# Kernel tuning notes

Hardware: AMD Instinct MI355X
Metric: run time of the kernel (lower is better)

## Reference

```python
import jax, jax.numpy as jnp
import numpy as np

B, N, NC, D, H = 2, 8192, 512, 512, 16
HD = D // H            # 32
SCALE = HD ** -0.5
EPS = 1e-6


def setup_inputs() -> dict:
    key = jax.random.key(0)
    k0, k1, k2, k3, k4 = jax.random.split(key, 5)
    return {
        "x": jax.random.normal(k0, (B, N, D), dtype=jnp.float32),
        "clusters": jax.random.normal(k1, (B, NC, D), dtype=jnp.float32),
        "Wq": jax.random.normal(k2, (D, D), dtype=jnp.float32) * 0.02,
        "Wkv": jax.random.normal(k3, (D, 2 * D), dtype=jnp.float32) * 0.02,
        "Wout": jax.random.normal(k4, (D, D), dtype=jnp.float32) * 0.02,
    }


def reference(x, clusters, Wq, Wkv, Wout):
    # projections (torch Linear without bias == matmul with weight)
    q = clusters @ Wq                      # [b, nc, d]
    kv = x @ Wkv                           # [b, n, 2d]
    # split heads: 'b n (h d) -> b h n d' and 'b n (k h d) -> k b h n d'
    q = q.reshape(B, NC, H, HD).transpose(0, 2, 1, 3)        # [b, h, nc, hd]
    kv = kv.reshape(B, N, 2, H, HD)
    k = kv[:, :, 0].transpose(0, 2, 1, 3)                    # [b, h, n, hd]
    v = kv[:, :, 1].transpose(0, 2, 1, 3)                    # [b, h, n, hd]

    attn = jnp.einsum('bhqd,bhkd->bhqk', q, k) * SCALE       # [b, h, nc, n]
    # 'soft' assignment: softmax over the CLUSTER (query) axis, dim=-2
    attn = jax.nn.softmax(attn, axis=-2)
    token_sizes = attn.sum(-1)                               # [b, h, nc]
    attn = attn / (token_sizes[..., None] + EPS)
    token_sizes = token_sizes.mean(axis=1)                   # [b, nc]

    out = jnp.einsum('bhqk,bhkd->bhqd', attn, v)             # [b, h, nc, hd]
    out = out.transpose(0, 2, 1, 3).reshape(B, NC, D)        # [b, nc, d]
    out = out @ Wout
    return out, token_sizes
```

## Files before the change

### kernel.cpp

```cpp
#include <hip/hip_runtime.h>
#include <hip/hip_bf16.h>

#define B_ 2
#define N_ 8192
#define NC_ 512
#define D_ 512
#define H_ 16
#define HD_ 32
#define SCALE_ 0.17677669529663687f
#define LOG2E_ 1.4426950408889634f
#define EPS_ 1e-6f
#define NCHUNK 32
#define CHUNK (N_ / NCHUNK)

typedef __attribute__((ext_vector_type(8))) short bf16x8_t;
typedef __attribute__((ext_vector_type(4))) short bf16x4_t;
typedef __attribute__((ext_vector_type(4))) float f32x4_t;

static __device__ __forceinline__ short f2bf(float f) {
    unsigned u = __float_as_uint(f);
    unsigned r = (u + 0x7FFFu + ((u >> 16) & 1u)) >> 16;
    return (short)r;
}

static __device__ __forceinline__ float fast_exp2(float x) {
#if __has_builtin(__builtin_amdgcn_exp2f)
    return __builtin_amdgcn_exp2f(x);
#else
    float r; asm("v_exp_f32 %0, %1" : "=v"(r) : "v"(x)); return r;
#endif
}

static __device__ __forceinline__ unsigned pack_trunc(float lo, float hi) {
    return __builtin_amdgcn_perm(__float_as_uint(hi), __float_as_uint(lo), 0x07060302u);
}

static __device__ __forceinline__ float bf2f(short s) {
    return __uint_as_float((unsigned)(unsigned short)s << 16);
}

static __device__ __forceinline__ void gload_lds16(const short* g, void* l) {
    __builtin_amdgcn_global_load_lds(
        (const __attribute__((address_space(1))) void*)g,
        (__attribute__((address_space(3))) void*)l, 16, 0, 0);
}

__global__ __launch_bounds__(256) void prep_kernel(
    const float* __restrict__ x, short* __restrict__ x_bf, int na8,
    const float* __restrict__ clusters, short* __restrict__ cl_bf,
    const float* __restrict__ Wq, const float* __restrict__ Wkv,
    const float* __restrict__ Wout,
    short* __restrict__ WqT, short* __restrict__ WkvT, short* __restrict__ WoutT)
{
    __shared__ short t[32][34];
    const int bid = blockIdx.x;
    if (bid < 4352) {
        int i8 = bid * 256 + threadIdx.x;
        const float* src; short* dst;
        if (i8 < na8) { src = x + (size_t)i8 * 8; dst = x_bf + (size_t)i8 * 8; }
        else { size_t o = (size_t)(i8 - na8) * 8; src = clusters + o; dst = cl_bf + o; }
        float4 v0 = *(const float4*)src;
        float4 v1 = *(const float4*)(src + 4);
        bf16x8_t p = {f2bf(v0.x), f2bf(v0.y), f2bf(v0.z), f2bf(v0.w),
                      f2bf(v1.x), f2bf(v1.y), f2bf(v1.z), f2bf(v1.w)};
        *(bf16x8_t*)dst = p;
        return;
    }
    const int idx = bid - 4352;
    const int bz = idx >> 9, rem = idx & 511;
    const int byy = rem >> 5, bxx = rem & 31;
    const float* src; short* dst; int ncols;
    if (bz == 0)      { src = Wq;   dst = WqT;   ncols = 512; }
    else if (bz == 1) { src = Wkv;  dst = WkvT;  ncols = 1024; }
    else              { src = Wout; dst = WoutT; ncols = 512; }
    if (bxx * 32 >= ncols) return;

    const int c0 = bxx * 32, r0 = byy * 32;
    const int tc = threadIdx.x & 31, tr = threadIdx.x >> 5;
#pragma unroll
    for (int i = 0; i < 4; i++) {
        int r = tr + i * 8;
        t[tc][r] = f2bf(src[(size_t)(r0 + r) * ncols + c0 + tc]);
    }
    __syncthreads();
#pragma unroll
    for (int i = 0; i < 4; i++) {
        int outr = tr + i * 8;
        dst[(size_t)(c0 + outr) * 512 + r0 + tc] = t[outr][tc];
    }
}

__global__ __launch_bounds__(256) void gemm_kvq_kernel(
    const short* __restrict__ x_bf, const short* __restrict__ WkvT,
    short* __restrict__ kvb,
    const short* __restrict__ cl_bf, const short* __restrict__ WqT,
    short* __restrict__ qb)
{
    __shared__ short As[2][128 * 32];
    __shared__ short Bs[2][128 * 32];

    const int tid = threadIdx.x;
    const int wid = tid >> 6, lane = tid & 63;
    const int l16 = lane & 15, lg = lane >> 4;
    const int wr = (wid >> 1) * 64, wc = (wid & 1) * 64;
    const int K = D_;

    const short* A; const short* BT; short* C; int N; float oscale; int bx, by;
    if (blockIdx.x < 1024) {
        int swz = (blockIdx.x & 7) * 128 + (blockIdx.x >> 3);
        bx = swz & 7; by = swz >> 3;
        A = x_bf; BT = WkvT; C = kvb; N = 2 * D_; oscale = 1.0f;
    } else {
        int r = blockIdx.x - 1024;
        bx = r & 3; by = r >> 2;
        A = cl_bf; BT = WqT; C = qb; N = D_; oscale = SCALE_ * LOG2E_;
    }

    const f32x4_t zero4 = {0.f, 0.f, 0.f, 0.f};
    f32x4_t acc[4][4];
#pragma unroll
    for (int i = 0; i < 4; i++)
#pragma unroll
        for (int j = 0; j < 4; j++) acc[i][j] = zero4;

    const short* aptr = A + (size_t)(by * 128 + wid * 16 + (lane >> 2)) * K + (lane & 3) * 8;
    const short* bptr = BT + (size_t)(bx * 128 + wid * 16 + (lane >> 2)) * K + (lane & 3) * 8;
    char* al0 = (char*)As[0] + wid * 1024;
    char* al1 = (char*)As[1] + wid * 1024;
    char* bl0 = (char*)Bs[0] + wid * 1024;
    char* bl1 = (char*)Bs[1] + wid * 1024;
    const size_t rstep = (size_t)64 * K;

    for (int kt = 0; kt < K; kt += 64) {
        gload_lds16(aptr + kt, al0);
        gload_lds16(aptr + rstep + kt, al0 + 4096);
        gload_lds16(aptr + kt + 32, al1);
        gload_lds16(aptr + rstep + kt + 32, al1 + 4096);
        gload_lds16(bptr + kt, bl0);
        gload_lds16(bptr + rstep + kt, bl0 + 4096);
        gload_lds16(bptr + kt + 32, bl1);
        gload_lds16(bptr + rstep + kt + 32, bl1 + 4096);
        __syncthreads();

#pragma unroll
        for (int sub = 0; sub < 2; sub++) {
            bf16x8_t bfr[4];
#pragma unroll
            for (int nf = 0; nf < 4; nf++)
                bfr[nf] = *(const bf16x8_t*)&Bs[sub][(wc + nf * 16 + l16) * 32 + lg * 8];
#pragma unroll
            for (int mf = 0; mf < 4; mf++) {
                bf16x8_t afr = *(const bf16x8_t*)&As[sub][(wr + mf * 16 + l16) * 32 + lg * 8];
#pragma unroll
                for (int nf = 0; nf < 4; nf++)
                    acc[mf][nf] = __builtin_amdgcn_mfma_f32_16x16x32_bf16(
                        afr, bfr[nf], acc[mf][nf], 0, 0, 0);
            }
        }
        __syncthreads();
    }

#pragma unroll
    for (int mf = 0; mf < 4; mf++) {
#pragma unroll
        for (int nf = 0; nf < 4; nf++) {
            int row0 = by * 128 + wr + mf * 16 + lg * 4;
            int col  = bx * 128 + wc + nf * 16 + l16;
#pragma unroll
            for (int r = 0; r < 4; r++)
                C[(size_t)(row0 + r) * N + col] = f2bf(acc[mf][nf][r] * oscale);
        }
    }
}

__global__ __launch_bounds__(256) void gemm_out_kernel(
    const short* __restrict__ A, const short* __restrict__ BT,
    float* __restrict__ C)
{
    __shared__ short As[2][128 * 32];
    __shared__ short Bs[2][128 * 32];

    const int tid = threadIdx.x;
    const int wid = tid >> 6, lane = tid & 63;
    const int l16 = lane & 15, lg = lane >> 4;
    const int wr = (wid >> 1) * 64, wc = (wid & 1) * 64;
    const int K = D_, N = D_;

    const int nwg = gridDim.x * gridDim.y;
    const int flat = blockIdx.y * gridDim.x + blockIdx.x;
    const int swz = (flat & 7) * (nwg >> 3) + (flat >> 3);
    const int bx = swz % gridDim.x, by = swz / gridDim.x;

    const f32x4_t zero4 = {0.f, 0.f, 0.f, 0.f};
    f32x4_t acc[4][4];
#pragma unroll
    for (int i = 0; i < 4; i++)
#pragma unroll
        for (int j = 0; j < 4; j++) acc[i][j] = zero4;

    const short* aptr = A + (size_t)(by * 128 + wid * 16 + (lane >> 2)) * K + (lane & 3) * 8;
    const short* bptr = BT + (size_t)(bx * 128 + wid * 16 + (lane >> 2)) * K + (lane & 3) * 8;
    char* al0 = (char*)As[0] + wid * 1024;
    char* al1 = (char*)As[1] + wid * 1024;
    char* bl0 = (char*)Bs[0] + wid * 1024;
    char* bl1 = (char*)Bs[1] + wid * 1024;
    const size_t rstep = (size_t)64 * K;

    for (int kt = 0; kt < K; kt += 64) {
        gload_lds16(aptr + kt, al0);
        gload_lds16(aptr + rstep + kt, al0 + 4096);
        gload_lds16(aptr + kt + 32, al1);
        gload_lds16(aptr + rstep + kt + 32, al1 + 4096);
        gload_lds16(bptr + kt, bl0);
        gload_lds16(bptr + rstep + kt, bl0 + 4096);
        gload_lds16(bptr + kt + 32, bl1);
        gload_lds16(bptr + rstep + kt + 32, bl1 + 4096);
        __syncthreads();

#pragma unroll
        for (int sub = 0; sub < 2; sub++) {
            bf16x8_t bfr[4];
#pragma unroll
            for (int nf = 0; nf < 4; nf++)
                bfr[nf] = *(const bf16x8_t*)&Bs[sub][(wc + nf * 16 + l16) * 32 + lg * 8];
#pragma unroll
            for (int mf = 0; mf < 4; mf++) {
                bf16x8_t afr = *(const bf16x8_t*)&As[sub][(wr + mf * 16 + l16) * 32 + lg * 8];
#pragma unroll
                for (int nf = 0; nf < 4; nf++)
                    acc[mf][nf] = __builtin_amdgcn_mfma_f32_16x16x32_bf16(
                        afr, bfr[nf], acc[mf][nf], 0, 0, 0);
            }
        }
        __syncthreads();
    }

#pragma unroll
    for (int mf = 0; mf < 4; mf++) {
#pragma unroll
        for (int nf = 0; nf < 4; nf++) {
            int row0 = by * 128 + wr + mf * 16 + lg * 4;
            int col  = bx * 128 + wc + nf * 16 + l16;
#pragma unroll
            for (int r = 0; r < 4; r++)
                C[(size_t)(row0 + r) * N + col] = acc[mf][nf][r];
        }
    }
}

__global__ __launch_bounds__(256) void attn_kernel(
    const short* __restrict__ qb,
    const short* __restrict__ kvb,
    short* __restrict__ out_part,
    float* __restrict__ ts_part)
{
    const int chunk = blockIdx.x, h = blockIdx.y, b = blockIdx.z;
    const int tid = threadIdx.x, wid = tid >> 6, lane = tid & 63;
    const int l16 = lane & 15, lg = lane >> 4;

    __shared__ short P_lds[512 * 32];
    __shared__ short v_t[2][32][40];
    __shared__ float reds[2][4][32];

    bf16x8_t qf[8];
#pragma unroll
    for (int mf = 0; mf < 8; mf++) {
        int row = wid * 128 + mf * 16 + l16;
        qf[mf] = *(const bf16x8_t*)&qb[(size_t)(b * NC_ + row) * D_ + h * HD_ + lg * 8];
    }

    const f32x4_t zero4 = {0.f, 0.f, 0.f, 0.f};
    f32x4_t oacc[8][2], tsacc[8];
#pragma unroll
    for (int mf = 0; mf < 8; mf++) {
        oacc[mf][0] = zero4; oacc[mf][1] = zero4; tsacc[mf] = zero4;
    }

    const short* kptr = kvb + (size_t)(b * N_ + chunk * CHUNK + l16) * (2 * D_) + h * HD_ + lg * 8;
    const int skey = tid >> 3, sd0 = (tid & 7) * 4;
    const short* vptr = kvb + (size_t)(b * N_ + chunk * CHUNK + skey) * (2 * D_) + D_ + h * HD_ + sd0;
    char* Pb = (char*)P_lds;

    bf16x8_t kf0 = *(const bf16x8_t*)(kptr);
    bf16x8_t kf1 = *(const bf16x8_t*)(kptr + 16 * (2 * D_));
    bf16x4_t vv  = *(const bf16x4_t*)(vptr);

    for (int kt = 0; kt < CHUNK / 32; kt++) {
        const int cur = kt & 1;

        v_t[cur][sd0 + 0][skey] = vv[0];
        v_t[cur][sd0 + 1][skey] = vv[1];
        v_t[cur][sd0 + 2][skey] = vv[2];
        v_t[cur][sd0 + 3][skey] = vv[3];

#pragma unroll
        for (int half = 0; half < 2; half++) {
            f32x4_t s[8];
            bf16x8_t kf = half ? kf1 : kf0;
#pragma unroll
            for (int mf = 0; mf < 8; mf++)
                s[mf] = __builtin_amdgcn_mfma_f32_16x16x32_bf16(qf[mf], kf, zero4, 0, 0, 0);

            const int kbyte = (l16 & 7) * 2;
            const int ku = (l16 >> 3) + half * 2;
            float sl = 0.f;
#pragma unroll
            for (int mf = 0; mf < 8; mf++) {
#pragma unroll
                for (int r = 0; r < 4; r++) {
                    float e = fast_exp2(s[mf][r]);
                    sl += e;
                    int row = wid * 128 + mf * 16 + lg * 4 + r;
                    int x = (row >> 1) & 3;
                    *(short*)(Pb + row * 64 + kbyte + (((ku ^ x) & 3) << 4)) =
                        (short)(__float_as_uint(e) >> 16);
                }
            }
            sl += __shfl_xor(sl, 16, 64);
            sl += __shfl_xor(sl, 32, 64);
            if (lane < 16) reds[cur][wid][half * 16 + lane] = sl;
        }

        {
            const size_t koffn = (size_t)((kt + 1) & (CHUNK / 32 - 1)) * 32 * (2 * D_);
            kf0 = *(const bf16x8_t*)(kptr + koffn);
            kf1 = *(const bf16x8_t*)(kptr + koffn + 16 * (2 * D_));
            vv  = *(const bf16x4_t*)(vptr + koffn);
        }

        __syncthreads();

        f32x4_t ta = *(const f32x4_t*)&reds[cur][0][lg * 8];
        f32x4_t tb = *(const f32x4_t*)&reds[cur][0][lg * 8 + 4];
#pragma unroll
        for (int w = 1; w < 4; w++) {
            ta += *(const f32x4_t*)&reds[cur][w][lg * 8];
            tb += *(const f32x4_t*)&reds[cur][w][lg * 8 + 4];
        }
        float iv[8];
#pragma unroll
        for (int r = 0; r < 4; r++) {
            iv[r]     = __fdividef(1.f, ta[r]);
            iv[4 + r] = __fdividef(1.f, tb[r]);
        }

        bf16x8_t v0r = *(const bf16x8_t*)&v_t[cur][l16][lg * 8];
        bf16x8_t v1r = *(const bf16x8_t*)&v_t[cur][16 + l16][lg * 8];
        bf16x8_t v0, v1, invf;
        {
            unsigned* p0 = (unsigned*)&v0;
            unsigned* p1 = (unsigned*)&v1;
            unsigned* pi = (unsigned*)&invf;
#pragma unroll
            for (int j = 0; j < 4; j++) {
                float a0 = bf2f(v0r[2 * j])     * iv[2 * j];
                float a1 = bf2f(v0r[2 * j + 1]) * iv[2 * j + 1];
                float b0 = bf2f(v1r[2 * j])     * iv[2 * j];
                float b1 = bf2f(v1r[2 * j + 1]) * iv[2 * j + 1];
                p0[j] = pack_trunc(a0, a1);
                p1[j] = pack_trunc(b0, b1);
                pi[j] = pack_trunc(iv[2 * j], iv[2 * j + 1]);
            }
        }

#pragma unroll
        for (int mf = 0; mf < 8; mf++) {
            int row = wid * 128 + mf * 16 + l16;
            bf16x8_t pa = *(const bf16x8_t*)(Pb + row * 64 +
                              (((lg ^ ((row >> 1) & 3)) & 3) << 4));
            oacc[mf][0] = __builtin_amdgcn_mfma_f32_16x16x32_bf16(pa, v0, oacc[mf][0], 0, 0, 0);
            oacc[mf][1] = __builtin_amdgcn_mfma_f32_16x16x32_bf16(pa, v1, oacc[mf][1], 0, 0, 0);
            tsacc[mf]   = __builtin_amdgcn_mfma_f32_16x16x32_bf16(pa, invf, tsacc[mf], 0, 0, 0);
        }
    }

    const size_t base = ((size_t)(chunk * B_ + b) * H_ + h);
#pragma unroll
    for (int mf = 0; mf < 8; mf++) {
        int row0 = wid * 128 + mf * 16 + lg * 4;
#pragma unroll
        for (int nf = 0; nf < 2; nf++) {
            int col = nf * 16 + l16;
#pragma unroll
            for (int r = 0; r < 4; r++)
                out_part[(base * NC_ + row0 + r) * HD_ + col] = f2bf(oacc[mf][nf][r]);
        }
        if (l16 == 0) {
#pragma unroll
            for (int r = 0; r < 4; r++)
                ts_part[base * NC_ + row0 + r] = tsacc[mf][r];
        }
    }
}

__global__ __launch_bounds__(256) void reduce_kernel(
    const short* __restrict__ out_part, const float* __restrict__ ts_part,
    short* __restrict__ out_mid, float* __restrict__ tok_out)
{
    const int bnc = blockIdx.x;
    const int b = bnc >> 9, nc = bnc & 511;
    const int t = threadIdx.x;
    __shared__ float tsh[16];
    if (t < 16) {
        float s = 0.f;
#pragma unroll
        for (int ch = 0; ch < NCHUNK; ch++)
            s += ts_part[((size_t)(ch * B_ + b) * H_ + t) * NC_ + nc];
        tsh[t] = s;
    }
    __syncthreads();
    if (t == 0) {
        float s = 0.f;
#pragma unroll
        for (int i = 0; i < 16; i++) s += tsh[i];
        tok_out[b * NC_ + nc] = s * (1.f / 16.f);
    }
    for (int c = t; c < D_; c += 256) {
        int hh = c >> 5, d = c & 31;
        float s = 0.f;
#pragma unroll
        for (int ch = 0; ch < NCHUNK; ch++) {
            unsigned short u = (unsigned short)
                out_part[(((size_t)(ch * B_ + b) * H_ + hh) * NC_ + nc) * HD_ + d];
            s += __uint_as_float((unsigned)u << 16);
        }
        out_mid[(size_t)(b * NC_ + nc) * D_ + c] = f2bf(s / (tsh[hh] + EPS_));
    }
}

extern "C" void kernel_launch(void* const* d_in, const int* in_sizes, int n_in,
                              void* d_out, int out_size, void* d_ws, size_t ws_size,
                              hipStream_t stream)
{
    (void)in_sizes; (void)n_in; (void)out_size; (void)ws_size;
    const float* x        = (const float*)d_in[0];
    const float* clusters = (const float*)d_in[1];
    const float* Wq       = (const float*)d_in[2];
    const float* Wkv      = (const float*)d_in[3];
    const float* Wout     = (const float*)d_in[4];

    char* ws = (char*)d_ws;
    short* x_bf     = (short*)(ws);
    short* WkvT     = (short*)(ws + 16777216);
    short* cl_bf    = (short*)(ws + 17825792);
    short* WqT      = (short*)(ws + 18874368);
    short* out_part = (short*)(ws);
    float* ts_part  = (float*)(ws + 33554432);
    short* kvb      = (short*)(ws + 35651584);
    short* out_mid  = (short*)(ws + 35651584);
    short* qb       = (short*)(ws + 69206016);
    short* WoutT    = (short*)(ws + 70254592);

    float* out = (float*)d_out;
    float* tok = out + (size_t)B_ * NC_ * D_;

    prep_kernel<<<dim3(5888), dim3(256), 0, stream>>>(
        x, x_bf, (B_ * N_ * D_) / 8, clusters, cl_bf,
        Wq, Wkv, Wout, WqT, WkvT, WoutT);
    gemm_kvq_kernel<<<dim3(1056), dim3(256), 0, stream>>>(
        x_bf, WkvT, kvb, cl_bf, WqT, qb);
    attn_kernel<<<dim3(NCHUNK, H_, B_), dim3(256), 0, stream>>>(
        qb, kvb, out_part, ts_part);
    reduce_kernel<<<dim3(B_ * NC_), dim3(256), 0, stream>>>(
        out_part, ts_part, out_mid, tok);
    gemm_out_kernel<<<dim3(D_ / 128, (B_ * NC_) / 128), dim3(256), 0, stream>>>(
        out_mid, WoutT, (float*)d_out);
}
```

Measured before the change: 118.7 us.

## Fuse fp32-to-bf16 conversion of x and clusters into the KV/Q GEMM loader

Removes the separate pass that converted x and clusters to bf16 in the prep kernel. The projection GEMM now loads fp32 activations straight into registers, converts them with v_cvt_pk_bf16_f32 and stores them to an XOR-swizzled LDS tile. The next K-step is prefetched into registers while the current one is computed. This drops a full write and reread of the 16 MB bf16 copy of x, in exchange for more fp32 global traffic inside the GEMM, higher register pressure and a conversion mode that may round differently.

```diff
diff --git a/kernel.cpp b/kernel.cpp
--- a/kernel.cpp
+++ b/kernel.cpp
@@ -16,6 +16,7 @@
 typedef __attribute__((ext_vector_type(8))) short bf16x8_t;
 typedef __attribute__((ext_vector_type(4))) short bf16x4_t;
 typedef __attribute__((ext_vector_type(4))) float f32x4_t;
+typedef __attribute__((ext_vector_type(2))) unsigned int u32x2_t;
 
 static __device__ __forceinline__ short f2bf(float f) {
     unsigned u = __float_as_uint(f);
@@ -35,6 +36,12 @@
     return __builtin_amdgcn_perm(__float_as_uint(hi), __float_as_uint(lo), 0x07060302u);
 }
 
+static __device__ __forceinline__ unsigned cvt_pk_bf16(float lo, float hi) {
+    unsigned r;
+    asm("v_cvt_pk_bf16_f32 %0, %1, %2" : "=v"(r) : "v"(lo), "v"(hi));
+    return r;
+}
+
 static __device__ __forceinline__ float bf2f(short s) {
     return __uint_as_float((unsigned)(unsigned short)s << 16);
 }
@@ -46,28 +53,12 @@
 }
 
 __global__ __launch_bounds__(256) void prep_kernel(
-    const float* __restrict__ x, short* __restrict__ x_bf, int na8,
-    const float* __restrict__ clusters, short* __restrict__ cl_bf,
     const float* __restrict__ Wq, const float* __restrict__ Wkv,
     const float* __restrict__ Wout,
     short* __restrict__ WqT, short* __restrict__ WkvT, short* __restrict__ WoutT)
 {
     __shared__ short t[32][34];
-    const int bid = blockIdx.x;
-    if (bid < 4352) {
-        int i8 = bid * 256 + threadIdx.x;
-        const float* src; short* dst;
-        if (i8 < na8) { src = x + (size_t)i8 * 8; dst = x_bf + (size_t)i8 * 8; }
-        else { size_t o = (size_t)(i8 - na8) * 8; src = clusters + o; dst = cl_bf + o; }
-        float4 v0 = *(const float4*)src;
-        float4 v1 = *(const float4*)(src + 4);
-        bf16x8_t p = {f2bf(v0.x), f2bf(v0.y), f2bf(v0.z), f2bf(v0.w),
-                      f2bf(v1.x), f2bf(v1.y), f2bf(v1.z), f2bf(v1.w)};
-        *(bf16x8_t*)dst = p;
-        return;
-    }
-    const int idx = bid - 4352;
-    const int bz = idx >> 9, rem = idx & 511;
+    const int bz = blockIdx.x >> 9, rem = blockIdx.x & 511;
     const int byy = rem >> 5, bxx = rem & 31;
     const float* src; short* dst; int ncols;
     if (bz == 0)      { src = Wq;   dst = WqT;   ncols = 512; }
@@ -91,9 +82,9 @@
 }
 
 __global__ __launch_bounds__(256) void gemm_kvq_kernel(
-    const short* __restrict__ x_bf, const short* __restrict__ WkvT,
+    const float* __restrict__ x, const short* __restrict__ WkvT,
     short* __restrict__ kvb,
-    const short* __restrict__ cl_bf, const short* __restrict__ WqT,
+    const float* __restrict__ clusters, const short* __restrict__ WqT,
     short* __restrict__ qb)
 {
     __shared__ short As[2][128 * 32];
@@ -105,15 +96,15 @@
     const int wr = (wid >> 1) * 64, wc = (wid & 1) * 64;
     const int K = D_;
 
-    const short* A; const short* BT; short* C; int N; float oscale; int bx, by;
+    const float* A; const short* BT; short* C; int N; float oscale; int bx, by;
     if (blockIdx.x < 1024) {
         int swz = (blockIdx.x & 7) * 128 + (blockIdx.x >> 3);
         bx = swz & 7; by = swz >> 3;
-        A = x_bf; BT = WkvT; C = kvb; N = 2 * D_; oscale = 1.0f;
+        A = x; BT = WkvT; C = kvb; N = 2 * D_; oscale = 1.0f;
     } else {
         int r = blockIdx.x - 1024;
         bx = r & 3; by = r >> 2;
-        A = cl_bf; BT = WqT; C = qb; N = D_; oscale = SCALE_ * LOG2E_;
+        A = clusters; BT = WqT; C = qb; N = D_; oscale = SCALE_ * LOG2E_;
     }
 
     const f32x4_t zero4 = {0.f, 0.f, 0.f, 0.f};
@@ -123,23 +114,41 @@
 #pragma unroll
         for (int j = 0; j < 4; j++) acc[i][j] = zero4;
 
-    const short* aptr = A + (size_t)(by * 128 + wid * 16 + (lane >> 2)) * K + (lane & 3) * 8;
+    const int sarow = tid >> 4;
+    const int scol4 = tid & 15;
+    const int ssub  = scol4 >> 3;
+    const int sconst = ((((scol4 & 7) >> 1) ^ ((sarow >> 1) & 3)) << 4) + (scol4 & 1) * 8;
+    const float* aload = A + (size_t)(by * 128 + sarow) * K + scol4 * 4;
+    char* sdst = (char*)As[ssub] + sarow * 64 + sconst;
+
     const short* bptr = BT + (size_t)(bx * 128 + wid * 16 + (lane >> 2)) * K + (lane & 3) * 8;
-    char* al0 = (char*)As[0] + wid * 1024;
-    char* al1 = (char*)As[1] + wid * 1024;
     char* bl0 = (char*)Bs[0] + wid * 1024;
     char* bl1 = (char*)Bs[1] + wid * 1024;
     const size_t rstep = (size_t)64 * K;
 
+    float4 curf[8];
+#pragma unroll
+    for (int k = 0; k < 8; k++)
+        curf[k] = *(const float4*)(aload + (size_t)(k * 16) * K);
+
     for (int kt = 0; kt < K; kt += 64) {
-        gload_lds16(aptr + kt, al0);
-        gload_lds16(aptr + rstep + kt, al0 + 4096);
-        gload_lds16(aptr + kt + 32, al1);
-        gload_lds16(aptr + rstep + kt + 32, al1 + 4096);
+#pragma unroll
+        for (int k = 0; k < 8; k++) {
+            u32x2_t w;
+            w[0] = cvt_pk_bf16(curf[k].x, curf[k].y);
+            w[1] = cvt_pk_bf16(curf[k].z, curf[k].w);
+            *(u32x2_t*)(sdst + k * 16 * 64) = w;
+        }
         gload_lds16(bptr + kt, bl0);
         gload_lds16(bptr + rstep + kt, bl0 + 4096);
         gload_lds16(bptr + kt + 32, bl1);
         gload_lds16(bptr + rstep + kt + 32, bl1 + 4096);
+        {
+            int ktn = (kt + 64 < K) ? (kt + 64) : 0;
+#pragma unroll
+            for (int k = 0; k < 8; k++)
+                curf[k] = *(const float4*)(aload + ktn + (size_t)(k * 16) * K);
+        }
         __syncthreads();
 
 #pragma unroll
@@ -150,7 +159,9 @@
                 bfr[nf] = *(const bf16x8_t*)&Bs[sub][(wc + nf * 16 + l16) * 32 + lg * 8];
 #pragma unroll
             for (int mf = 0; mf < 4; mf++) {
-                bf16x8_t afr = *(const bf16x8_t*)&As[sub][(wr + mf * 16 + l16) * 32 + lg * 8];
+                int arow = wr + mf * 16 + l16;
+                bf16x8_t afr = *(const bf16x8_t*)((char*)As[sub] + arow * 64 +
+                                   (((lg ^ ((arow >> 1) & 3)) & 3) << 4));
 #pragma unroll
                 for (int nf = 0; nf < 4; nf++)
                     acc[mf][nf] = __builtin_amdgcn_mfma_f32_16x16x32_bf16(
@@ -440,9 +451,7 @@
     const float* Wout     = (const float*)d_in[4];
 
     char* ws = (char*)d_ws;
-    short* x_bf     = (short*)(ws);
     short* WkvT     = (short*)(ws + 16777216);
-    short* cl_bf    = (short*)(ws + 17825792);
     short* WqT      = (short*)(ws + 18874368);
     short* out_part = (short*)(ws);
     float* ts_part  = (float*)(ws + 33554432);
@@ -454,11 +463,10 @@
     float* out = (float*)d_out;
     float* tok = out + (size_t)B_ * NC_ * D_;
 
-    prep_kernel<<<dim3(5888), dim3(256), 0, stream>>>(
-        x, x_bf, (B_ * N_ * D_) / 8, clusters, cl_bf,
+    prep_kernel<<<dim3(1536), dim3(256), 0, stream>>>(
         Wq, Wkv, Wout, WqT, WkvT, WoutT);
     gemm_kvq_kernel<<<dim3(1056), dim3(256), 0, stream>>>(
-        x_bf, WkvT, kvb, cl_bf, WqT, qb);
+        x, WkvT, kvb, clusters, WqT, qb);
     attn_kernel<<<dim3(NCHUNK, H_, B_), dim3(256), 0, stream>>>(
         qb, kvb, out_part, ts_part);
     reduce_kernel<<<dim3(B_ * NC_), dim3(256), 0, stream>>>(
```

Result: slower. 125.1 us (+5.4%).
